# Optimization experiments

Hardware: AMD Instinct MI355X
Metric: run time of the kernel (lower is better)

Reference implementation:

```python
import jax, jax.numpy as jnp
import numpy as np

SEQ, DM, STATE, BATCH = 1024, 512, 16, 8
D2 = 2 * DM
EPS = 1e-5


def rmsnorm(x, w):
    return x * jax.lax.rsqrt(jnp.mean(x * x, axis=-1, keepdims=True) + EPS) * w


def setup_inputs() -> dict:
    key = jax.random.key(0)
    ks = jax.random.split(key, 16)
    def lin(k, i, o):
        k1, k2 = jax.random.split(k)
        s = 1.0 / np.sqrt(i)
        return (jax.random.uniform(k1, (i, o), minval=-s, maxval=s),
                jax.random.uniform(k2, (o,), minval=-s, maxval=s))
    inp_w, inp_b = lin(ks[0], DM, D2)
    convlin_w, convlin_b = lin(ks[1], D2, D2)
    fc1_w, fc1_b = lin(ks[2], D2, D2)
    fc2_w, fc2_b = lin(ks[3], D2, STATE)
    fc3_w, fc3_b = lin(ks[4], D2, STATE)
    D_w, D_b = lin(ks[5], DM, D2)
    out_w, _ = lin(ks[6], D2, DM)
    out_b = jnp.ones((DM,))  # nn.init.constant_(out_proj.bias, 1.0)
    # Conv1d(seq_len, seq_len, k=3): weight (out_ch=SEQ, in_ch=SEQ, 3)
    s = 1.0 / np.sqrt(SEQ * 3)
    conv_w = jax.random.uniform(ks[7], (SEQ, SEQ, 3), minval=-s, maxval=s)
    conv_b = jax.random.uniform(ks[8], (SEQ,), minval=-s, maxval=s)
    norm_w = jnp.ones((DM,))
    x = jax.random.normal(ks[9], (BATCH, SEQ, DM))
    return dict(x=x, norm_w=norm_w, inp_w=inp_w, inp_b=inp_b, conv_w=conv_w,
                conv_b=conv_b, convlin_w=convlin_w, convlin_b=convlin_b,
                fc1_w=fc1_w, fc1_b=fc1_b, fc2_w=fc2_w, fc2_b=fc2_b,
                fc3_w=fc3_w, fc3_b=fc3_b, D_w=D_w, D_b=D_b,
                out_w=out_w, out_b=out_b)


def reference(x, norm_w, inp_w, inp_b, conv_w, conv_b, convlin_w, convlin_b,
              fc1_w, fc1_b, fc2_w, fc2_b, fc3_w, fc3_b, D_w, D_b, out_w, out_b):
    xn = rmsnorm(x, norm_w)                                  # (b, L, d)
    x_proj = xn @ inp_w + inp_b                              # (b, L, 2d)
    # Conv1d over channels=seq_len, spatial=2d, padding=1
    x_conv = jax.lax.conv_general_dilated(
        x_proj, conv_w, window_strides=(1,), padding=[(1, 1)],
        dimension_numbers=('NCH', 'OIH', 'NCH')) + conv_b[None, :, None]
    x_conv_out = jax.nn.silu(x_conv) @ convlin_w + convlin_b  # (b, L, 2d)
    # S6: h starts at zero so dA term vanishes; y = x*delta*sum_n(B*C)
    u = x_conv_out
    B = u @ fc2_w + fc2_b                                     # (b, L, n)
    C = u @ fc3_w + fc3_b                                     # (b, L, n)
    delta = jax.nn.softplus(u @ fc1_w + fc1_b)                # (b, L, 2d)
    bc = jnp.sum(B * C, axis=-1, keepdims=True)               # (b, L, 1)
    x_ssm = u * delta * bc                                    # (b, L, 2d)
    x_act = jax.nn.silu(x_ssm)
    x_residual = jax.nn.silu(xn @ D_w + D_b)
    return (x_residual * x_act) @ out_w + out_b               # (b, L, d)
```

## Files before the change

kernel.cpp:

```cpp
#include <hip/hip_runtime.h>
#include <hip/hip_bf16.h>

#define SEQ 1024
#define DM 512
#define D2 1024
#define NSTATE 16
#define BATCH 8
#define ROWS (BATCH * SEQ)
#define EPSF 1e-5f

typedef __attribute__((ext_vector_type(8))) short bf16x8;
typedef __attribute__((ext_vector_type(4))) float f32x4;

#define AS1 __attribute__((address_space(1)))
#define AS3 __attribute__((address_space(3)))

__device__ __forceinline__ void gll16(const void* g, void* l) {
    __builtin_amdgcn_global_load_lds(
        (const AS1 unsigned int*)(uintptr_t)g,
        (AS3 unsigned int*)(unsigned int)(uintptr_t)l, 16, 0, 0);
}

__device__ __forceinline__ float sigmoidf_(float x) {
    return 1.f / (1.f + __expf(-x));
}
__device__ __forceinline__ unsigned short f2bf(float f) {
    __hip_bfloat16 h = __float2bfloat16(f);
    unsigned short r;
    __builtin_memcpy(&r, &h, 2);
    return r;
}

__global__ __launch_bounds__(256) void tcvt_k(const float* __restrict__ src,
                                              __hip_bfloat16* __restrict__ dst,
                                              int R, int C) {
    __shared__ float tile[32][33];
    int c0 = blockIdx.x * 32, r0 = blockIdx.y * 32;
    int tx = threadIdx.x & 31, ty = threadIdx.x >> 5;
#pragma unroll
    for (int p = 0; p < 4; ++p) {
        int r = r0 + ty + p * 8, c = c0 + tx;
        if (r < R && c < C) tile[ty + p * 8][tx] = src[(size_t)r * C + c];
    }
    __syncthreads();
#pragma unroll
    for (int p = 0; p < 4; ++p) {
        int c = c0 + ty + p * 8, r = r0 + tx;
        if (r < R && c < C)
            dst[(size_t)c * R + r] = __float2bfloat16(tile[tx][ty + p * 8]);
    }
}

__global__ __launch_bounds__(256) void convw_k(const float* __restrict__ cw,
                                               __hip_bfloat16* __restrict__ wk) {
    int idx = blockIdx.x * 256 + threadIdx.x;
    float a = cw[(size_t)idx * 3 + 0];
    float b = cw[(size_t)idx * 3 + 1];
    float c = cw[(size_t)idx * 3 + 2];
    wk[idx] = __float2bfloat16(a);
    wk[(size_t)SEQ * SEQ + idx] = __float2bfloat16(b);
    wk[(size_t)2 * SEQ * SEQ + idx] = __float2bfloat16(c);
}

__global__ __launch_bounds__(256) void rmsnorm_k(
    const float* __restrict__ x, const float* __restrict__ w,
    __hip_bfloat16* __restrict__ o) {
    int row = blockIdx.x;
    const float* xr = x + (size_t)row * DM;
    __hip_bfloat16* orow = o + (size_t)row * DM;
    int t = threadIdx.x;
    float v0 = xr[t];
    float v1 = xr[t + 256];
    float ss = v0 * v0 + v1 * v1;
#pragma unroll
    for (int off = 32; off; off >>= 1) ss += __shfl_down(ss, off, 64);
    __shared__ float parts[4];
    if ((t & 63) == 0) parts[t >> 6] = ss;
    __syncthreads();
    float tot = parts[0] + parts[1] + parts[2] + parts[3];
    float rs = rsqrtf(tot * (1.f / DM) + EPSF);
    orow[t] = __float2bfloat16(v0 * rs * w[t]);
    orow[t + 256] = __float2bfloat16(v1 * rs * w[t + 256]);
}

template <int EPI>
__global__ __launch_bounds__(256) void mgemm(
    const __hip_bfloat16* __restrict__ A, const __hip_bfloat16* __restrict__ Bt,
    const float* __restrict__ bias, void* __restrict__ outp,
    void* __restrict__ outp2, const float* __restrict__ bias2,
    const __hip_bfloat16* __restrict__ uptr,
    const __hip_bfloat16* __restrict__ resid, const float* __restrict__ bcv,
    int M, int N, int K) {
    __shared__ __align__(16) __hip_bfloat16 As[3][128 * 32];
    __shared__ __align__(16) __hip_bfloat16 Bs[3][128 * 32];
    const int nbx = gridDim.x;
    int lin = blockIdx.y * nbx + blockIdx.x;
    int chunk = (nbx * gridDim.y) >> 3;
    int wg = (lin & 7) * chunk + (lin >> 3);
    const int n0 = (wg % nbx) * 128, m0 = (wg / nbx) * 128;
    const int t = threadIdx.x, lane = t & 63, w = t >> 6;
    const int wr = w >> 1, wc = w & 1;
    const int l15 = lane & 15, l4 = lane >> 4;

    const int r0_ = t >> 2, c0_ = (t & 3) ^ ((r0_ >> 1) & 3);
    const int b1 = 256 + t, r1_ = b1 >> 2, c1_ = (b1 & 3) ^ ((r1_ >> 1) & 3);
    const __hip_bfloat16* gA0 = A + (size_t)(m0 + r0_) * K + c0_ * 8;
    const __hip_bfloat16* gA1 = A + (size_t)(m0 + r1_) * K + c1_ * 8;
    const __hip_bfloat16* gB0 = Bt + (size_t)(n0 + r0_) * K + c0_ * 8;
    const __hip_bfloat16* gB1 = Bt + (size_t)(n0 + r1_) * K + c1_ * 8;
    const int d0 = (w * 64) * 8, d1 = (256 + w * 64) * 8;

    int offA[4], offB[4];
#pragma unroll
    for (int i = 0; i < 4; ++i) {
        int ra = wr * 64 + i * 16 + l15;
        offA[i] = (ra * 4 + (l4 ^ ((ra >> 1) & 3))) * 8;
        int rb = wc * 64 + i * 16 + l15;
        offB[i] = (rb * 4 + (l4 ^ ((rb >> 1) & 3))) * 8;
    }

#define MSTAGE(BUF, K0)                  \
    {                                    \
        gll16(gA0 + (K0), &As[BUF][d0]); \
        gll16(gA1 + (K0), &As[BUF][d1]); \
        gll16(gB0 + (K0), &Bs[BUF][d0]); \
        gll16(gB1 + (K0), &Bs[BUF][d1]); \
    }

    f32x4 acc[4][4] = {};
    const int NT = K >> 5;
    unsigned curb = 0, nxtb = 1, thdb = 2;
    MSTAGE(0, 0);
    MSTAGE(1, 32);
    asm volatile("s_waitcnt vmcnt(4)" ::: "memory");
    __builtin_amdgcn_s_barrier();
    __builtin_amdgcn_sched_barrier(0);

#pragma unroll 1
    for (int kt = 0; kt < NT; ++kt) {
        const bool st = (kt + 2 < NT);
        if (st) MSTAGE(thdb, (kt + 2) * 32);
        bf16x8 af[4], bv[4];
#pragma unroll
        for (int i = 0; i < 4; ++i) {
            af[i] = *(const bf16x8*)&As[curb][offA[i]];
            bv[i] = *(const bf16x8*)&Bs[curb][offB[i]];
        }
#pragma unroll
        for (int i = 0; i < 4; ++i)
#pragma unroll
            for (int j = 0; j < 4; ++j)
                acc[i][j] = __builtin_amdgcn_mfma_f32_16x16x32_bf16(
                    af[i], bv[j], acc[i][j], 0, 0, 0);
        if (kt + 1 < NT) {
            if (st)
                asm volatile("s_waitcnt vmcnt(4)" ::: "memory");
            else
                asm volatile("s_waitcnt vmcnt(0)" ::: "memory");
            __builtin_amdgcn_s_barrier();
            __builtin_amdgcn_sched_barrier(0);
        }
        unsigned tb = curb;
        curb = nxtb;
        nxtb = thdb;
        thdb = tb;
    }
#undef MSTAGE

    const int mb = m0 + wr * 64, nb = n0 + wc * 64;
#pragma unroll
    for (int i = 0; i < 4; ++i) {
#pragma unroll
        for (int j = 0; j < 4; ++j) {
            int ngl = nb + j * 16 + l15;
            if (EPI == 5) {
                if (nb < D2) {
                    float bj = bias[ngl];
                    int b = m0 >> 10;
                    int ibase = (mb & (SEQ - 1)) + i * 16 + l4 * 4;
                    ushort4 pk;
                    pk.x = f2bf(acc[i][j][0] + bj);
                    pk.y = f2bf(acc[i][j][1] + bj);
                    pk.z = f2bf(acc[i][j][2] + bj);
                    pk.w = f2bf(acc[i][j][3] + bj);
                    *(ushort4*)((__hip_bfloat16*)outp +
                                ((size_t)b * D2 + ngl) * SEQ + ibase) = pk;
                } else {
                    int ng2 = ngl - D2;
                    float bj = bias2[ng2];
#pragma unroll
                    for (int r = 0; r < 4; ++r) {
                        int mg = mb + i * 16 + l4 * 4 + r;
                        float c = acc[i][j][r] + bj;
                        ((__hip_bfloat16*)outp2)[(size_t)mg * D2 + ng2] =
                            __float2bfloat16(c * sigmoidf_(c));
                    }
                }
            } else {
                float bj = bias[ngl];
#pragma unroll
                for (int r = 0; r < 4; ++r) {
                    int mg = mb + i * 16 + l4 * 4 + r;
                    size_t ro = (size_t)mg * N + ngl;
                    float c = acc[i][j][r] + bj;
                    if (EPI == 1) {
                        ((__hip_bfloat16*)outp)[ro] = __float2bfloat16(c);
                    } else if (EPI == 3) {
                        float sp = (c > 20.f) ? c : log1pf(__expf(c));
                        float xs = __bfloat162float(uptr[ro]) * sp * bcv[mg];
                        float v = __bfloat162float(resid[ro]) *
                                  (xs * sigmoidf_(xs));
                        ((__hip_bfloat16*)outp)[ro] = __float2bfloat16(v);
                    } else {
                        ((float*)outp)[ro] = c;
                    }
                }
            }
        }
    }
}

__global__ __launch_bounds__(256) void conv_mfma(
    const __hip_bfloat16* __restrict__ wk,
    const __hip_bfloat16* __restrict__ Xt,
    const float* __restrict__ cb, __hip_bfloat16* __restrict__ outp) {
    __shared__ __align__(16) __hip_bfloat16 Ws[2][3][128 * 32];
    __shared__ __align__(16) __hip_bfloat16 Xs[2][128 * 32];
    __shared__ __align__(16) __hip_bfloat16 Xh[2][SEQ];
    int lin = blockIdx.x + 8 * blockIdx.y + 64 * blockIdx.z;
    int wg = (lin & 7) * 64 + (lin >> 3);
    const int n0 = (wg & 7) * 128;
    const int m0 = ((wg >> 3) & 7) * 128;
    const int z = wg >> 6;
    const int t = threadIdx.x, lane = t & 63, w = t >> 6;
    const int wr = w >> 1, wc = w & 1;
    const int l15 = lane & 15, l4 = lane >> 4;
    const __hip_bfloat16* Xtb = Xt + (size_t)z * D2 * SEQ;

    {
        int which = t >> 7;
        int col = (t & 127) * 8;
        int h = n0 - 1 + which * 129;
        uint4 v = make_uint4(0u, 0u, 0u, 0u);
        if (h >= 0 && h < D2)
            v = *(const uint4*)(Xtb + (size_t)h * SEQ + col);
        *(uint4*)&Xh[which][col] = v;
    }

    int rowp[2], cbw[2];
#pragma unroll
    for (int p = 0; p < 2; ++p) {
        int blk = p * 256 + t;
        rowp[p] = blk >> 2;
        cbw[p] = (blk & 3) ^ ((rowp[p] >> 1) & 3);
    }
    const __hip_bfloat16* wsrc[2][3];
    const __hip_bfloat16* xsrc[2];
#pragma unroll
    for (int p = 0; p < 2; ++p) {
#pragma unroll
        for (int tp = 0; tp < 3; ++tp)
            wsrc[p][tp] = wk + (size_t)tp * SEQ * SEQ +
                          (size_t)(m0 + rowp[p]) * SEQ + cbw[p] * 8;
        xsrc[p] = Xtb + (size_t)(n0 + rowp[p]) * SEQ + cbw[p] * 8;
    }
    const int dst0 = (w * 64) * 8, dst1 = (256 + w * 64) * 8;

    int offA[4];
#pragma unroll
    for (int i = 0; i < 4; ++i) {
        int ra = wr * 64 + i * 16 + l15;
        offA[i] = (ra * 4 + (l4 ^ ((ra >> 1) & 3))) * 8;
    }

#define CSTAGE(BUF, K0)                              \
    {                                                \
        gll16(wsrc[0][0] + (K0), &Ws[BUF][0][dst0]); \
        gll16(wsrc[1][0] + (K0), &Ws[BUF][0][dst1]); \
        gll16(wsrc[0][1] + (K0), &Ws[BUF][1][dst0]); \
        gll16(wsrc[1][1] + (K0), &Ws[BUF][1][dst1]); \
        gll16(wsrc[0][2] + (K0), &Ws[BUF][2][dst0]); \
        gll16(wsrc[1][2] + (K0), &Ws[BUF][2][dst1]); \
        gll16(xsrc[0] + (K0), &Xs[BUF][dst0]);       \
        gll16(xsrc[1] + (K0), &Xs[BUF][dst1]);       \
    }

    f32x4 acc[4][4] = {};
    CSTAGE(0, 0);
    asm volatile("s_waitcnt vmcnt(0) lgkmcnt(0)" ::: "memory");
    __builtin_amdgcn_s_barrier();
    __builtin_amdgcn_sched_barrier(0);

#pragma unroll 1
    for (int kt = 0; kt < 32; ++kt) {
        const int k0 = kt * 32;
        const int buf = kt & 1;
        if (kt + 1 < 32) CSTAGE(buf ^ 1, (kt + 1) * 32);
        bf16x8 aw[3][4];
#pragma unroll
        for (int tp = 0; tp < 3; ++tp)
#pragma unroll
            for (int i = 0; i < 4; ++i)
                aw[tp][i] = *(const bf16x8*)&Ws[buf][tp][offA[i]];
#pragma unroll
        for (int j = 0; j < 4; ++j) {
#pragma unroll
            for (int tp = 0; tp < 3; ++tp) {
                int rb = wc * 64 + j * 16 + l15 + tp;
                int r = rb - 1;
                const __hip_bfloat16* src =
                    &Xs[buf][(r * 4 + (l4 ^ ((r >> 1) & 3))) * 8];
                if (rb == 0) src = &Xh[0][k0 + l4 * 8];
                if (rb == 129) src = &Xh[1][k0 + l4 * 8];
                bf16x8 bvx = *(const bf16x8*)src;
#pragma unroll
                for (int i = 0; i < 4; ++i)
                    acc[i][j] = __builtin_amdgcn_mfma_f32_16x16x32_bf16(
                        aw[tp][i], bvx, acc[i][j], 0, 0, 0);
            }
        }
        if (kt + 1 < 32) {
            asm volatile("s_waitcnt vmcnt(0)" ::: "memory");
            __builtin_amdgcn_s_barrier();
            __builtin_amdgcn_sched_barrier(0);
        }
    }
#undef CSTAGE

    const int mb = m0 + wr * 64, nb = n0 + wc * 64;
    size_t ob = (size_t)z * SEQ * D2;
#pragma unroll
    for (int i = 0; i < 4; ++i)
#pragma unroll
        for (int j = 0; j < 4; ++j)
#pragma unroll
            for (int r = 0; r < 4; ++r) {
                int mg = mb + i * 16 + l4 * 4 + r;
                int ng = nb + j * 16 + l15;
                float c = acc[i][j][r] + cb[mg];
                outp[ob + (size_t)mg * D2 + ng] =
                    __float2bfloat16(c * sigmoidf_(c));
            }
}

__global__ __launch_bounds__(256) void bc2_k(
    const __hip_bfloat16* __restrict__ u, const __hip_bfloat16* __restrict__ fcT,
    const float* __restrict__ b2, const float* __restrict__ b3,
    float* __restrict__ bc) {
    __shared__ __align__(16) __hip_bfloat16 Bl[32 * 1024];
    __shared__ __align__(16) __hip_bfloat16 As[3][128 * 32];
    const int m0 = blockIdx.x * 128;
    const int t = threadIdx.x, lane = t & 63, w = t >> 6;
    const int l15 = lane & 15, l4 = lane >> 4;

#pragma unroll
    for (int it = 0; it < 16; ++it) {
        int q = it * 256 + t;
        int n = q >> 7, blk = q & 127;
        uint4 v = *(const uint4*)(fcT + (size_t)n * 1024 + blk * 8);
        *(uint4*)&Bl[(n * 128 + (blk ^ (n & 7))) * 8] = v;
    }

    const int r0_ = t >> 2, c0_ = (t & 3) ^ ((r0_ >> 1) & 3);
    const int bq = 256 + t, r1_ = bq >> 2, c1_ = (bq & 3) ^ ((r1_ >> 1) & 3);
    const __hip_bfloat16* gA0 = u + (size_t)(m0 + r0_) * 1024 + c0_ * 8;
    const __hip_bfloat16* gA1 = u + (size_t)(m0 + r1_) * 1024 + c1_ * 8;
    const int d0 = (w * 64) * 8, d1 = (256 + w * 64) * 8;

    int offA[2];
#pragma unroll
    for (int i = 0; i < 2; ++i) {
        int ra = w * 32 + i * 16 + l15;
        offA[i] = (ra * 4 + (l4 ^ ((ra >> 1) & 3))) * 8;
    }

#define BSTAGE(BUF, K0)                  \
    {                                    \
        gll16(gA0 + (K0), &As[BUF][d0]); \
        gll16(gA1 + (K0), &As[BUF][d1]); \
    }

    f32x4 acc[2][2] = {};
    unsigned curb = 0, nxtb = 1, thdb = 2;
    BSTAGE(0, 0);
    BSTAGE(1, 32);
    asm volatile("s_waitcnt vmcnt(2)" ::: "memory");
    __builtin_amdgcn_s_barrier();
    __builtin_amdgcn_sched_barrier(0);

#pragma unroll 1
    for (int kt = 0; kt < 32; ++kt) {
        const bool st = (kt + 2 < 32);
        if (st) BSTAGE(thdb, (kt + 2) * 32);
        bf16x8 af[2], bf[2];
#pragma unroll
        for (int i = 0; i < 2; ++i) af[i] = *(const bf16x8*)&As[curb][offA[i]];
#pragma unroll
        for (int nj = 0; nj < 2; ++nj) {
            int n = nj * 16 + l15;
            int blk = (kt * 4 + l4) ^ (n & 7);
            bf[nj] = *(const bf16x8*)&Bl[(n * 128 + blk) * 8];
        }
#pragma unroll
        for (int i = 0; i < 2; ++i)
#pragma unroll
            for (int nj = 0; nj < 2; ++nj)
                acc[i][nj] = __builtin_amdgcn_mfma_f32_16x16x32_bf16(
                    af[i], bf[nj], acc[i][nj], 0, 0, 0);
        if (kt + 1 < 32) {
            if (st)
                asm volatile("s_waitcnt vmcnt(2)" ::: "memory");
            else
                asm volatile("s_waitcnt vmcnt(0)" ::: "memory");
            __builtin_amdgcn_s_barrier();
            __builtin_amdgcn_sched_barrier(0);
        }
        unsigned tb = curb;
        curb = nxtb;
        nxtb = thdb;
        thdb = tb;
    }
#undef BSTAGE

    float bb2 = b2[l15], bb3 = b3[l15];
#pragma unroll
    for (int i = 0; i < 2; ++i)
#pragma unroll
        for (int r = 0; r < 4; ++r) {
            float Bv = acc[i][0][r] + bb2;
            float Cv = acc[i][1][r] + bb3;
            float p = Bv * Cv;
            p += __shfl_xor(p, 1, 64);
            p += __shfl_xor(p, 2, 64);
            p += __shfl_xor(p, 4, 64);
            p += __shfl_xor(p, 8, 64);
            if (l15 == 0)
                bc[m0 + w * 32 + i * 16 + l4 * 4 + r] = p;
        }
}

extern "C" void kernel_launch(void* const* d_in, const int* in_sizes, int n_in,
                              void* d_out, int out_size, void* d_ws,
                              size_t ws_size, hipStream_t stream) {
    const float* x = (const float*)d_in[0];
    const float* norm_w = (const float*)d_in[1];
    const float* inp_w = (const float*)d_in[2];
    const float* inp_b = (const float*)d_in[3];
    const float* conv_w = (const float*)d_in[4];
    const float* conv_b = (const float*)d_in[5];
    const float* convlin_w = (const float*)d_in[6];
    const float* convlin_b = (const float*)d_in[7];
    const float* fc1_w = (const float*)d_in[8];
    const float* fc1_b = (const float*)d_in[9];
    const float* fc2_w = (const float*)d_in[10];
    const float* fc2_b = (const float*)d_in[11];
    const float* fc3_w = (const float*)d_in[12];
    const float* fc3_b = (const float*)d_in[13];
    const float* D_w = (const float*)d_in[14];
    const float* D_b = (const float*)d_in[15];
    const float* out_w = (const float*)d_in[16];
    const float* out_b = (const float*)d_in[17];
    float* out = (float*)d_out;

    __hip_bfloat16* xnb = (__hip_bfloat16*)d_ws;
    __hip_bfloat16* xt = xnb + (size_t)ROWS * DM;
    __hip_bfloat16* cvo = xt + (size_t)BATCH * D2 * SEQ;
    __hip_bfloat16* u = cvo + (size_t)ROWS * D2;
    __hip_bfloat16* resid = u + (size_t)ROWS * D2;
    __hip_bfloat16* Wcat = resid + (size_t)ROWS * D2;
    __hip_bfloat16* clT = Wcat + (size_t)2 * D2 * DM;
    __hip_bfloat16* fc1T = clT + (size_t)D2 * D2;
    __hip_bfloat16* outT = fc1T + (size_t)D2 * D2;
    __hip_bfloat16* wk = outT + (size_t)DM * D2;
    __hip_bfloat16* fcT = wk + (size_t)3 * SEQ * SEQ;
    float* bcb = (float*)(fcT + (size_t)32 * D2);

    tcvt_k<<<dim3(D2 / 32, DM / 32), 256, 0, stream>>>(inp_w, Wcat, DM, D2);
    tcvt_k<<<dim3(D2 / 32, DM / 32), 256, 0, stream>>>(
        D_w, Wcat + (size_t)D2 * DM, DM, D2);
    tcvt_k<<<dim3(D2 / 32, D2 / 32), 256, 0, stream>>>(convlin_w, clT, D2, D2);
    tcvt_k<<<dim3(D2 / 32, D2 / 32), 256, 0, stream>>>(fc1_w, fc1T, D2, D2);
    tcvt_k<<<dim3(DM / 32, D2 / 32), 256, 0, stream>>>(out_w, outT, D2, DM);
    tcvt_k<<<dim3(1, D2 / 32), 256, 0, stream>>>(fc2_w, fcT, D2, NSTATE);
    tcvt_k<<<dim3(1, D2 / 32), 256, 0, stream>>>(fc3_w, fcT + (size_t)16 * D2,
                                                 D2, NSTATE);
    convw_k<<<SEQ * SEQ / 256, 256, 0, stream>>>(conv_w, wk);
    rmsnorm_k<<<ROWS, 256, 0, stream>>>(x, norm_w, xnb);
    mgemm<5><<<dim3(2 * D2 / 128, ROWS / 128), 256, 0, stream>>>(
        xnb, Wcat, inp_b, xt, resid, D_b, nullptr, nullptr, nullptr, ROWS,
        2 * D2, DM);
    conv_mfma<<<dim3(D2 / 128, SEQ / 128, BATCH), 256, 0, stream>>>(
        wk, xt, conv_b, cvo);
    mgemm<1><<<dim3(D2 / 128, ROWS / 128), 256, 0, stream>>>(
        cvo, clT, convlin_b, u, nullptr, nullptr, nullptr, nullptr, nullptr,
        ROWS, D2, D2);
    bc2_k<<<ROWS / 128, 256, 0, stream>>>(u, fcT, fc2_b, fc3_b, bcb);
    mgemm<3><<<dim3(D2 / 128, ROWS / 128), 256, 0, stream>>>(
        u, fc1T, fc1_b, cvo, nullptr, nullptr, u, resid, bcb, ROWS, D2, D2);
    mgemm<4><<<dim3(DM / 128, ROWS / 128), 256, 0, stream>>>(
        cvo, outT, out_b, out, nullptr, nullptr, nullptr, nullptr, nullptr,
        ROWS, DM, D2);
}
```

Measured before the change: 241.9 us.

## Shrink GEMM and conv tiles to 64 rows and split the fused input projection

The main GEMM kernel and the conv MFMA kernel move from 128x128 tiles to 64x128, doubling the number of workgroups and halving per-thread accumulators, so more of the GPU's compute units have work and occupancy can rise. The fused input/D projection is split into two GEMMs. The input projection is now computed as a transposed product (weights times activations), so its output lands directly in the transposed layout the conv needs, replacing the packed scattered-store epilogue. The cost is less data reuse per tile and one extra kernel launch.

Result: slower. 257.7 us (+6.5%).

```diff
diff --git a/kernel.cpp b/kernel.cpp
--- a/kernel.cpp
+++ b/kernel.cpp
@@ -23,12 +23,6 @@
 
 __device__ __forceinline__ float sigmoidf_(float x) {
     return 1.f / (1.f + __expf(-x));
-}
-__device__ __forceinline__ unsigned short f2bf(float f) {
-    __hip_bfloat16 h = __float2bfloat16(f);
-    unsigned short r;
-    __builtin_memcpy(&r, &h, 2);
-    return r;
 }
 
 __global__ __launch_bounds__(256) void tcvt_k(const float* __restrict__ src,
@@ -87,52 +81,52 @@
 __global__ __launch_bounds__(256) void mgemm(
     const __hip_bfloat16* __restrict__ A, const __hip_bfloat16* __restrict__ Bt,
     const float* __restrict__ bias, void* __restrict__ outp,
-    void* __restrict__ outp2, const float* __restrict__ bias2,
     const __hip_bfloat16* __restrict__ uptr,
     const __hip_bfloat16* __restrict__ resid, const float* __restrict__ bcv,
     int M, int N, int K) {
-    __shared__ __align__(16) __hip_bfloat16 As[3][128 * 32];
+    __shared__ __align__(16) __hip_bfloat16 As[3][64 * 32];
     __shared__ __align__(16) __hip_bfloat16 Bs[3][128 * 32];
     const int nbx = gridDim.x;
     int lin = blockIdx.y * nbx + blockIdx.x;
     int chunk = (nbx * gridDim.y) >> 3;
     int wg = (lin & 7) * chunk + (lin >> 3);
-    const int n0 = (wg % nbx) * 128, m0 = (wg / nbx) * 128;
+    const int n0 = (wg % nbx) * 128, m0 = (wg / nbx) * 64;
     const int t = threadIdx.x, lane = t & 63, w = t >> 6;
     const int wr = w >> 1, wc = w & 1;
     const int l15 = lane & 15, l4 = lane >> 4;
 
-    const int r0_ = t >> 2, c0_ = (t & 3) ^ ((r0_ >> 1) & 3);
-    const int b1 = 256 + t, r1_ = b1 >> 2, c1_ = (b1 & 3) ^ ((r1_ >> 1) & 3);
-    const __hip_bfloat16* gA0 = A + (size_t)(m0 + r0_) * K + c0_ * 8;
-    const __hip_bfloat16* gA1 = A + (size_t)(m0 + r1_) * K + c1_ * 8;
-    const __hip_bfloat16* gB0 = Bt + (size_t)(n0 + r0_) * K + c0_ * 8;
-    const __hip_bfloat16* gB1 = Bt + (size_t)(n0 + r1_) * K + c1_ * 8;
+    const int rA = t >> 2, cA = (t & 3) ^ ((rA >> 1) & 3);
+    const int b1 = 256 + t, rB1 = b1 >> 2, cB1 = (b1 & 3) ^ ((rB1 >> 1) & 3);
+    const __hip_bfloat16* gA = A + (size_t)(m0 + rA) * K + cA * 8;
+    const __hip_bfloat16* gB0 = Bt + (size_t)(n0 + rA) * K + cA * 8;
+    const __hip_bfloat16* gB1 = Bt + (size_t)(n0 + rB1) * K + cB1 * 8;
     const int d0 = (w * 64) * 8, d1 = (256 + w * 64) * 8;
 
-    int offA[4], offB[4];
-#pragma unroll
-    for (int i = 0; i < 4; ++i) {
-        int ra = wr * 64 + i * 16 + l15;
+    int offA[2], offB[4];
+#pragma unroll
+    for (int i = 0; i < 2; ++i) {
+        int ra = wr * 32 + i * 16 + l15;
         offA[i] = (ra * 4 + (l4 ^ ((ra >> 1) & 3))) * 8;
-        int rb = wc * 64 + i * 16 + l15;
-        offB[i] = (rb * 4 + (l4 ^ ((rb >> 1) & 3))) * 8;
+    }
+#pragma unroll
+    for (int j = 0; j < 4; ++j) {
+        int rb = wc * 64 + j * 16 + l15;
+        offB[j] = (rb * 4 + (l4 ^ ((rb >> 1) & 3))) * 8;
     }
 
 #define MSTAGE(BUF, K0)                  \
     {                                    \
-        gll16(gA0 + (K0), &As[BUF][d0]); \
-        gll16(gA1 + (K0), &As[BUF][d1]); \
+        gll16(gA + (K0), &As[BUF][d0]);  \
         gll16(gB0 + (K0), &Bs[BUF][d0]); \
         gll16(gB1 + (K0), &Bs[BUF][d1]); \
     }
 
-    f32x4 acc[4][4] = {};
+    f32x4 acc[2][4] = {};
     const int NT = K >> 5;
     unsigned curb = 0, nxtb = 1, thdb = 2;
     MSTAGE(0, 0);
     MSTAGE(1, 32);
-    asm volatile("s_waitcnt vmcnt(4)" ::: "memory");
+    asm volatile("s_waitcnt vmcnt(3)" ::: "memory");
     __builtin_amdgcn_s_barrier();
     __builtin_amdgcn_sched_barrier(0);
 
@@ -140,21 +134,20 @@
     for (int kt = 0; kt < NT; ++kt) {
         const bool st = (kt + 2 < NT);
         if (st) MSTAGE(thdb, (kt + 2) * 32);
-        bf16x8 af[4], bv[4];
-#pragma unroll
-        for (int i = 0; i < 4; ++i) {
-            af[i] = *(const bf16x8*)&As[curb][offA[i]];
-            bv[i] = *(const bf16x8*)&Bs[curb][offB[i]];
-        }
-#pragma unroll
-        for (int i = 0; i < 4; ++i)
+        bf16x8 af[2], bv[4];
+#pragma unroll
+        for (int i = 0; i < 2; ++i) af[i] = *(const bf16x8*)&As[curb][offA[i]];
+#pragma unroll
+        for (int j = 0; j < 4; ++j) bv[j] = *(const bf16x8*)&Bs[curb][offB[j]];
+#pragma unroll
+        for (int i = 0; i < 2; ++i)
 #pragma unroll
             for (int j = 0; j < 4; ++j)
                 acc[i][j] = __builtin_amdgcn_mfma_f32_16x16x32_bf16(
                     af[i], bv[j], acc[i][j], 0, 0, 0);
         if (kt + 1 < NT) {
             if (st)
-                asm volatile("s_waitcnt vmcnt(4)" ::: "memory");
+                asm volatile("s_waitcnt vmcnt(3)" ::: "memory");
             else
                 asm volatile("s_waitcnt vmcnt(0)" ::: "memory");
             __builtin_amdgcn_s_barrier();
@@ -167,34 +160,21 @@
     }
 #undef MSTAGE
 
-    const int mb = m0 + wr * 64, nb = n0 + wc * 64;
-#pragma unroll
-    for (int i = 0; i < 4; ++i) {
+    const int mb = m0 + wr * 32, nb = n0 + wc * 64;
+#pragma unroll
+    for (int i = 0; i < 2; ++i) {
 #pragma unroll
         for (int j = 0; j < 4; ++j) {
             int ngl = nb + j * 16 + l15;
-            if (EPI == 5) {
-                if (nb < D2) {
-                    float bj = bias[ngl];
-                    int b = m0 >> 10;
-                    int ibase = (mb & (SEQ - 1)) + i * 16 + l4 * 4;
-                    ushort4 pk;
-                    pk.x = f2bf(acc[i][j][0] + bj);
-                    pk.y = f2bf(acc[i][j][1] + bj);
-                    pk.z = f2bf(acc[i][j][2] + bj);
-                    pk.w = f2bf(acc[i][j][3] + bj);
-                    *(ushort4*)((__hip_bfloat16*)outp +
-                                ((size_t)b * D2 + ngl) * SEQ + ibase) = pk;
-                } else {
-                    int ng2 = ngl - D2;
-                    float bj = bias2[ng2];
-#pragma unroll
-                    for (int r = 0; r < 4; ++r) {
-                        int mg = mb + i * 16 + l4 * 4 + r;
-                        float c = acc[i][j][r] + bj;
-                        ((__hip_bfloat16*)outp2)[(size_t)mg * D2 + ng2] =
-                            __float2bfloat16(c * sigmoidf_(c));
-                    }
+            if (EPI == 6) {
+                int bz = ngl >> 10, tl = ngl & 1023;
+#pragma unroll
+                for (int r = 0; r < 4; ++r) {
+                    int mg = mb + i * 16 + l4 * 4 + r;
+                    float c = acc[i][j][r] + bias[mg];
+                    ((__hip_bfloat16*)outp)[(size_t)bz * D2 * SEQ +
+                                            (size_t)mg * SEQ + tl] =
+                        __float2bfloat16(c);
                 }
             } else {
                 float bj = bias[ngl];
@@ -205,6 +185,9 @@
                     float c = acc[i][j][r] + bj;
                     if (EPI == 1) {
                         ((__hip_bfloat16*)outp)[ro] = __float2bfloat16(c);
+                    } else if (EPI == 2) {
+                        ((__hip_bfloat16*)outp)[ro] =
+                            __float2bfloat16(c * sigmoidf_(c));
                     } else if (EPI == 3) {
                         float sp = (c > 20.f) ? c : log1pf(__expf(c));
                         float xs = __bfloat162float(uptr[ro]) * sp * bcv[mg];
@@ -224,14 +207,14 @@
     const __hip_bfloat16* __restrict__ wk,
     const __hip_bfloat16* __restrict__ Xt,
     const float* __restrict__ cb, __hip_bfloat16* __restrict__ outp) {
-    __shared__ __align__(16) __hip_bfloat16 Ws[2][3][128 * 32];
+    __shared__ __align__(16) __hip_bfloat16 Ws[2][3][64 * 32];
     __shared__ __align__(16) __hip_bfloat16 Xs[2][128 * 32];
     __shared__ __align__(16) __hip_bfloat16 Xh[2][SEQ];
-    int lin = blockIdx.x + 8 * blockIdx.y + 64 * blockIdx.z;
-    int wg = (lin & 7) * 64 + (lin >> 3);
+    int lin = blockIdx.x + 8 * blockIdx.y + 128 * blockIdx.z;
+    int wg = (lin & 7) * 128 + (lin >> 3);
     const int n0 = (wg & 7) * 128;
-    const int m0 = ((wg >> 3) & 7) * 128;
-    const int z = wg >> 6;
+    const int m0 = ((wg >> 3) & 15) * 64;
+    const int z = wg >> 7;
     const int t = threadIdx.x, lane = t & 63, w = t >> 6;
     const int wr = w >> 1, wc = w & 1;
     const int l15 = lane & 15, l4 = lane >> 4;
@@ -247,45 +230,34 @@
         *(uint4*)&Xh[which][col] = v;
     }
 
-    int rowp[2], cbw[2];
-#pragma unroll
-    for (int p = 0; p < 2; ++p) {
-        int blk = p * 256 + t;
-        rowp[p] = blk >> 2;
-        cbw[p] = (blk & 3) ^ ((rowp[p] >> 1) & 3);
-    }
-    const __hip_bfloat16* wsrc[2][3];
-    const __hip_bfloat16* xsrc[2];
-#pragma unroll
-    for (int p = 0; p < 2; ++p) {
-#pragma unroll
-        for (int tp = 0; tp < 3; ++tp)
-            wsrc[p][tp] = wk + (size_t)tp * SEQ * SEQ +
-                          (size_t)(m0 + rowp[p]) * SEQ + cbw[p] * 8;
-        xsrc[p] = Xtb + (size_t)(n0 + rowp[p]) * SEQ + cbw[p] * 8;
-    }
-    const int dst0 = (w * 64) * 8, dst1 = (256 + w * 64) * 8;
-
-    int offA[4];
-#pragma unroll
-    for (int i = 0; i < 4; ++i) {
-        int ra = wr * 64 + i * 16 + l15;
+    const int rA = t >> 2, cA = (t & 3) ^ ((rA >> 1) & 3);
+    const int b1 = 256 + t, rB1 = b1 >> 2, cB1 = (b1 & 3) ^ ((rB1 >> 1) & 3);
+    const __hip_bfloat16* wsrc[3];
+#pragma unroll
+    for (int tp = 0; tp < 3; ++tp)
+        wsrc[tp] = wk + (size_t)tp * SEQ * SEQ + (size_t)(m0 + rA) * SEQ +
+                   cA * 8;
+    const __hip_bfloat16* xsrc0 = Xtb + (size_t)(n0 + rA) * SEQ + cA * 8;
+    const __hip_bfloat16* xsrc1 = Xtb + (size_t)(n0 + rB1) * SEQ + cB1 * 8;
+    const int d0 = (w * 64) * 8, d1 = (256 + w * 64) * 8;
+
+    int offA[2];
+#pragma unroll
+    for (int i = 0; i < 2; ++i) {
+        int ra = wr * 32 + i * 16 + l15;
         offA[i] = (ra * 4 + (l4 ^ ((ra >> 1) & 3))) * 8;
     }
 
-#define CSTAGE(BUF, K0)                              \
-    {                                                \
-        gll16(wsrc[0][0] + (K0), &Ws[BUF][0][dst0]); \
-        gll16(wsrc[1][0] + (K0), &Ws[BUF][0][dst1]); \
-        gll16(wsrc[0][1] + (K0), &Ws[BUF][1][dst0]); \
-        gll16(wsrc[1][1] + (K0), &Ws[BUF][1][dst1]); \
-        gll16(wsrc[0][2] + (K0), &Ws[BUF][2][dst0]); \
-        gll16(wsrc[1][2] + (K0), &Ws[BUF][2][dst1]); \
-        gll16(xsrc[0] + (K0), &Xs[BUF][dst0]);       \
-        gll16(xsrc[1] + (K0), &Xs[BUF][dst1]);       \
-    }
-
-    f32x4 acc[4][4] = {};
+#define CSTAGE(BUF, K0)                            \
+    {                                              \
+        gll16(wsrc[0] + (K0), &Ws[BUF][0][d0]);    \
+        gll16(wsrc[1] + (K0), &Ws[BUF][1][d0]);    \
+        gll16(wsrc[2] + (K0), &Ws[BUF][2][d0]);    \
+        gll16(xsrc0 + (K0), &Xs[BUF][d0]);         \
+        gll16(xsrc1 + (K0), &Xs[BUF][d1]);         \
+    }
+
+    f32x4 acc[2][4] = {};
     CSTAGE(0, 0);
     asm volatile("s_waitcnt vmcnt(0) lgkmcnt(0)" ::: "memory");
     __builtin_amdgcn_s_barrier();
@@ -296,11 +268,11 @@
         const int k0 = kt * 32;
         const int buf = kt & 1;
         if (kt + 1 < 32) CSTAGE(buf ^ 1, (kt + 1) * 32);
-        bf16x8 aw[3][4];
+        bf16x8 aw[3][2];
 #pragma unroll
         for (int tp = 0; tp < 3; ++tp)
 #pragma unroll
-            for (int i = 0; i < 4; ++i)
+            for (int i = 0; i < 2; ++i)
                 aw[tp][i] = *(const bf16x8*)&Ws[buf][tp][offA[i]];
 #pragma unroll
         for (int j = 0; j < 4; ++j) {
@@ -314,7 +286,7 @@
                 if (rb == 129) src = &Xh[1][k0 + l4 * 8];
                 bf16x8 bvx = *(const bf16x8*)src;
 #pragma unroll
-                for (int i = 0; i < 4; ++i)
+                for (int i = 0; i < 2; ++i)
                     acc[i][j] = __builtin_amdgcn_mfma_f32_16x16x32_bf16(
                         aw[tp][i], bvx, acc[i][j], 0, 0, 0);
             }
@@ -327,10 +299,10 @@
     }
 #undef CSTAGE
 
-    const int mb = m0 + wr * 64, nb = n0 + wc * 64;
+    const int mb = m0 + wr * 32, nb = n0 + wc * 64;
     size_t ob = (size_t)z * SEQ * D2;
 #pragma unroll
-    for (int i = 0; i < 4; ++i)
+    for (int i = 0; i < 2; ++i)
 #pragma unroll
         for (int j = 0; j < 4; ++j)
 #pragma unroll
@@ -467,17 +439,17 @@
     __hip_bfloat16* cvo = xt + (size_t)BATCH * D2 * SEQ;
     __hip_bfloat16* u = cvo + (size_t)ROWS * D2;
     __hip_bfloat16* resid = u + (size_t)ROWS * D2;
-    __hip_bfloat16* Wcat = resid + (size_t)ROWS * D2;
-    __hip_bfloat16* clT = Wcat + (size_t)2 * D2 * DM;
+    __hip_bfloat16* inpT = resid + (size_t)ROWS * D2;
+    __hip_bfloat16* DT = inpT + (size_t)D2 * DM;
+    __hip_bfloat16* clT = DT + (size_t)D2 * DM;
     __hip_bfloat16* fc1T = clT + (size_t)D2 * D2;
     __hip_bfloat16* outT = fc1T + (size_t)D2 * D2;
     __hip_bfloat16* wk = outT + (size_t)DM * D2;
     __hip_bfloat16* fcT = wk + (size_t)3 * SEQ * SEQ;
     float* bcb = (float*)(fcT + (size_t)32 * D2);
 
-    tcvt_k<<<dim3(D2 / 32, DM / 32), 256, 0, stream>>>(inp_w, Wcat, DM, D2);
-    tcvt_k<<<dim3(D2 / 32, DM / 32), 256, 0, stream>>>(
-        D_w, Wcat + (size_t)D2 * DM, DM, D2);
+    tcvt_k<<<dim3(D2 / 32, DM / 32), 256, 0, stream>>>(inp_w, inpT, DM, D2);
+    tcvt_k<<<dim3(D2 / 32, DM / 32), 256, 0, stream>>>(D_w, DT, DM, D2);
     tcvt_k<<<dim3(D2 / 32, D2 / 32), 256, 0, stream>>>(convlin_w, clT, D2, D2);
     tcvt_k<<<dim3(D2 / 32, D2 / 32), 256, 0, stream>>>(fc1_w, fc1T, D2, D2);
     tcvt_k<<<dim3(DM / 32, D2 / 32), 256, 0, stream>>>(out_w, outT, D2, DM);
@@ -486,18 +458,17 @@
                                                  D2, NSTATE);
     convw_k<<<SEQ * SEQ / 256, 256, 0, stream>>>(conv_w, wk);
     rmsnorm_k<<<ROWS, 256, 0, stream>>>(x, norm_w, xnb);
-    mgemm<5><<<dim3(2 * D2 / 128, ROWS / 128), 256, 0, stream>>>(
-        xnb, Wcat, inp_b, xt, resid, D_b, nullptr, nullptr, nullptr, ROWS,
-        2 * D2, DM);
-    conv_mfma<<<dim3(D2 / 128, SEQ / 128, BATCH), 256, 0, stream>>>(
+    mgemm<6><<<dim3(ROWS / 128, D2 / 64), 256, 0, stream>>>(
+        inpT, xnb, inp_b, xt, nullptr, nullptr, nullptr, D2, ROWS, DM);
+    mgemm<2><<<dim3(D2 / 128, ROWS / 64), 256, 0, stream>>>(
+        xnb, DT, D_b, resid, nullptr, nullptr, nullptr, ROWS, D2, DM);
+    conv_mfma<<<dim3(D2 / 128, SEQ / 64, BATCH), 256, 0, stream>>>(
         wk, xt, conv_b, cvo);
-    mgemm<1><<<dim3(D2 / 128, ROWS / 128), 256, 0, stream>>>(
-        cvo, clT, convlin_b, u, nullptr, nullptr, nullptr, nullptr, nullptr,
-        ROWS, D2, D2);
+    mgemm<1><<<dim3(D2 / 128, ROWS / 64), 256, 0, stream>>>(
+        cvo, clT, convlin_b, u, nullptr, nullptr, nullptr, ROWS, D2, D2);
     bc2_k<<<ROWS / 128, 256, 0, stream>>>(u, fcT, fc2_b, fc3_b, bcb);
-    mgemm<3><<<dim3(D2 / 128, ROWS / 128), 256, 0, stream>>>(
-        u, fc1T, fc1_b, cvo, nullptr, nullptr, u, resid, bcb, ROWS, D2, D2);
-    mgemm<4><<<dim3(DM / 128, ROWS / 128), 256, 0, stream>>>(
-        cvo, outT, out_b, out, nullptr, nullptr, nullptr, nullptr, nullptr,
-        ROWS, DM, D2);
-}
+    mgemm<3><<<dim3(D2 / 128, ROWS / 64), 256, 0, stream>>>(
+        u, fc1T, fc1_b, cvo, u, resid, bcb, ROWS, D2, D2);
+    mgemm<4><<<dim3(DM / 128, ROWS / 64), 256, 0, stream>>>(
+        cvo, outT, out_b, out, nullptr, nullptr, nullptr, ROWS, DM, D2);
+}
```
